# Kernel tuning notes

Measured on AMD Instinct MI355X. Metric: run time of the kernel, lower is better.

Reference implementation:

```python
import jax, jax.numpy as jnp
import numpy as np

BANDWIDTH = 0.001
THRESHOLD_INIT = 0.01


def setup_inputs() -> dict:
    key = jax.random.key(0)
    k1, k2, k3 = jax.random.split(key, 3)
    N, d_model, d_sae = 8192, 2048, 16384
    x = jax.random.normal(k1, (N, d_model), dtype=jnp.float32)
    # scale ~ 1/sqrt(d) so pre-activations are O(1) and threshold=0.01 gives sparsity
    W_enc = jax.random.normal(k2, (d_model, d_sae), dtype=jnp.float32) / np.sqrt(d_model)
    b_enc = jnp.zeros((d_sae,), dtype=jnp.float32)
    threshold = jnp.full((d_sae,), THRESHOLD_INIT, dtype=jnp.float32)
    W_dec = jax.random.normal(k3, (d_sae, d_model), dtype=jnp.float32) / np.sqrt(d_sae)
    b_dec = jnp.zeros((d_model,), dtype=jnp.float32)
    return {"x": x, "W_enc": W_enc, "b_enc": b_enc, "threshold": threshold,
            "W_dec": W_dec, "b_dec": b_dec}


def reference(x, W_enc, b_enc, threshold, W_dec, b_dec):
    # encode: F.linear(x - b_dec, W_enc.t(), b_enc) == (x - b_dec) @ W_enc + b_enc
    pre = (x - b_dec) @ W_enc + b_enc                      # [N, d_sae]
    mask = (pre > threshold).astype(pre.dtype)
    features = pre * mask                                   # JumpReLU
    # decode: features @ W_dec + b_dec
    reconstruction = features @ W_dec + b_dec               # [N, d_model]
    return (reconstruction, features)
```

## Files before the change

kernel.cpp:

```cpp
#include <hip/hip_runtime.h>
#include <hip/hip_bf16.h>


#define BM 128
#define BN 128
#define BK 32

typedef __bf16 bf16x8 __attribute__((ext_vector_type(8)));
typedef float  f32x4  __attribute__((ext_vector_type(4)));

__device__ __forceinline__ short f2bf(float f) {
    unsigned u = __float_as_uint(f);
    unsigned r = u + 0x7FFF + ((u >> 16) & 1);
    return (short)(r >> 16);
}

__device__ __forceinline__ void gl_lds16(const void* g, void* l) {
    __builtin_amdgcn_global_load_lds(
        (const __attribute__((address_space(1))) unsigned int*)g,
        (__attribute__((address_space(3))) unsigned int*)l, 16, 0, 0);
}

__global__ __launch_bounds__(256) void prep_x(const float* __restrict__ x,
                                              const float* __restrict__ b_dec,
                                              short* __restrict__ xb) {
    int idx = (blockIdx.x * 256 + threadIdx.x) * 4;
    float4 v = *(const float4*)(x + idx);
    int k = idx & 2047;
    float4 b = *(const float4*)(b_dec + k);
    short4 o;
    o.x = f2bf(v.x - b.x);
    o.y = f2bf(v.y - b.y);
    o.z = f2bf(v.z - b.z);
    o.w = f2bf(v.w - b.w);
    *(short4*)(xb + idx) = o;
}

__global__ __launch_bounds__(256) void transpose_cvt(const float* __restrict__ in,
                                                     short* __restrict__ out,
                                                     int R, int C) {
    __shared__ float tile[32][33];
    int c0 = blockIdx.x * 32;
    int r0 = blockIdx.y * 32;
    int tx = threadIdx.x, ty = threadIdx.y;
    for (int i = 0; i < 32; i += 8)
        tile[ty + i][tx] = in[(size_t)(r0 + ty + i) * C + (c0 + tx)];
    __syncthreads();
    for (int i = 0; i < 32; i += 8)
        out[(size_t)(c0 + ty + i) * R + (r0 + tx)] = f2bf(tile[tx][ty + i]);
}

__global__ __launch_bounds__(256) void gemm_bt(
    const short* __restrict__ A, const short* __restrict__ Bt,
    const float* __restrict__ bias, const float* __restrict__ thr,
    float* __restrict__ Cf, short* __restrict__ Cb,
    int M, int N, int K) {
    __shared__ short As[BM * BK];
    __shared__ short Bs[BN * BK];

    const int tid  = threadIdx.x;
    const int lane = tid & 63;
    const int wave = tid >> 6;
    const int wm = wave >> 1, wn = wave & 1;
    const int bm = blockIdx.x, bn = blockIdx.y;

    const short* Abase = A  + (size_t)bm * 128 * K;
    const short* Bbase = Bt + (size_t)bn * 128 * K;

    const int srow = lane >> 2;
    const int skof = (lane & 3) * 8;

    f32x4 acc[4][4];
#pragma unroll
    for (int mi = 0; mi < 4; mi++)
#pragma unroll
        for (int ni = 0; ni < 4; ni++)
            acc[mi][ni] = (f32x4){0.f, 0.f, 0.f, 0.f};

    const int mrow = lane & 15;
    const int kq   = (lane >> 4) * 8;

    for (int kt = 0; kt < K; kt += BK) {
#pragma unroll
        for (int i = 0; i < 2; i++) {
            int iid = wave + i * 4;
            int row = iid * 16 + srow;
            gl_lds16(Abase + (size_t)row * K + kt + skof, (char*)As + iid * 1024);
            gl_lds16(Bbase + (size_t)row * K + kt + skof, (char*)Bs + iid * 1024);
        }
        __syncthreads();

        bf16x8 af[4], bfr[4];
#pragma unroll
        for (int mi = 0; mi < 4; mi++)
            af[mi] = *(const bf16x8*)(As + (wm * 64 + mi * 16 + mrow) * BK + kq);
#pragma unroll
        for (int ni = 0; ni < 4; ni++)
            bfr[ni] = *(const bf16x8*)(Bs + (wn * 64 + ni * 16 + mrow) * BK + kq);
#pragma unroll
        for (int mi = 0; mi < 4; mi++)
#pragma unroll
            for (int ni = 0; ni < 4; ni++)
                acc[mi][ni] = __builtin_amdgcn_mfma_f32_16x16x32_bf16(
                    af[mi], bfr[ni], acc[mi][ni], 0, 0, 0);
        __syncthreads();
    }

    const int colbase = bn * 128 + wn * 64;
    const int rowbase = bm * 128 + wm * 64;
#pragma unroll
    for (int mi = 0; mi < 4; mi++) {
        int row0 = rowbase + mi * 16 + (lane >> 4) * 4;
#pragma unroll
        for (int ni = 0; ni < 4; ni++) {
            int col = colbase + ni * 16 + mrow;
            float bz = bias[col];
            float tz = thr ? thr[col] : 0.f;
#pragma unroll
            for (int r = 0; r < 4; r++) {
                float v = acc[mi][ni][r] + bz;
                if (thr) v = (v > tz) ? v : 0.f;
                size_t off = (size_t)(row0 + r) * N + col;
                Cf[off] = v;
                if (Cb) Cb[off] = f2bf(v);
            }
        }
    }
}

extern "C" void kernel_launch(void* const* d_in, const int* in_sizes, int n_in,
                              void* d_out, int out_size, void* d_ws, size_t ws_size,
                              hipStream_t stream) {
    const float* x      = (const float*)d_in[0];
    const float* W_enc  = (const float*)d_in[1];
    const float* b_enc  = (const float*)d_in[2];
    const float* thr    = (const float*)d_in[3];
    const float* W_dec  = (const float*)d_in[4];
    const float* b_dec  = (const float*)d_in[5];

    const int N = 8192, DM = 2048, DS = 16384;

    float* recon = (float*)d_out;
    float* feats = (float*)d_out + (size_t)N * DM;

    char* ws = (char*)d_ws;
    short* xb    = (short*)ws;
    short* wencT = (short*)(ws + ((size_t)32 << 20));
    short* wdecT = (short*)(ws + ((size_t)96 << 20));
    short* fb    = (short*)(ws + ((size_t)160 << 20));

    prep_x<<<(N * DM) / (256 * 4), 256, 0, stream>>>(x, b_dec, xb);
    transpose_cvt<<<dim3(DS / 32, DM / 32), dim3(32, 8), 0, stream>>>(W_enc, wencT, DM, DS);
    transpose_cvt<<<dim3(DM / 32, DS / 32), dim3(32, 8), 0, stream>>>(W_dec, wdecT, DS, DM);

    gemm_bt<<<dim3(N / 128, DS / 128), 256, 0, stream>>>(
        xb, wencT, b_enc, thr, feats, fb, N, DS, DM);
    gemm_bt<<<dim3(N / 128, DM / 128), 256, 0, stream>>>(
        fb, wdecT, b_dec, nullptr, recon, nullptr, N, DM, DS);
}
```

Before: 2.515 ms.

## Replace GEMM with 256x256 double-buffered swizzled 8-wave kernel and faster transpose

Replaces the 128x128 single-buffered GEMM with a 256x256-tile, 512-thread kernel. The new kernel uses a BK=64 double-buffered LDS pipeline, an XOR-swizzled LDS layout, staged prefetch interleaved with four MFMA phases, setprio, and a workgroup remap for L2 locality. The transpose now converts to bf16 before writing to LDS and stores packed short2 values. The aim is more data reuse per tile, hidden global-load latency and fewer LDS bank conflicts. In exchange, the GEMM uses heavy register pressure (one block per CU) and 128KB of LDS.

```diff
diff --git a/kernel.cpp b/kernel.cpp
--- a/kernel.cpp
+++ b/kernel.cpp
@@ -1,10 +1,6 @@
 #include <hip/hip_runtime.h>
 #include <hip/hip_bf16.h>
 
-
-#define BM 128
-#define BN 128
-#define BK 32
 
 typedef __bf16 bf16x8 __attribute__((ext_vector_type(8)));
 typedef float  f32x4  __attribute__((ext_vector_type(4)));
@@ -19,6 +15,12 @@
     __builtin_amdgcn_global_load_lds(
         (const __attribute__((address_space(1))) unsigned int*)g,
         (__attribute__((address_space(3))) unsigned int*)l, 16, 0, 0);
+}
+
+__device__ __forceinline__ void fence_bar() {
+    asm volatile("" ::: "memory");
+    __builtin_amdgcn_s_barrier();
+    asm volatile("" ::: "memory");
 }
 
 __global__ __launch_bounds__(256) void prep_x(const float* __restrict__ x,
@@ -36,91 +38,197 @@
     *(short4*)(xb + idx) = o;
 }
 
-__global__ __launch_bounds__(256) void transpose_cvt(const float* __restrict__ in,
-                                                     short* __restrict__ out,
-                                                     int R, int C) {
-    __shared__ float tile[32][33];
-    int c0 = blockIdx.x * 32;
-    int r0 = blockIdx.y * 32;
-    int tx = threadIdx.x, ty = threadIdx.y;
-    for (int i = 0; i < 32; i += 8)
-        tile[ty + i][tx] = in[(size_t)(r0 + ty + i) * C + (c0 + tx)];
+__global__ __launch_bounds__(256) void transpose_cvt64(const float* __restrict__ in,
+                                                       short* __restrict__ out,
+                                                       int R, int C) {
+    __shared__ short t[32][66];
+    const int tid = threadIdx.x;
+    const int c0 = blockIdx.x * 32;
+    const int r0 = blockIdx.y * 64;
+#pragma unroll
+    for (int i = 0; i < 8; ++i) {
+        int idx = tid + i * 256;
+        int r = idx >> 5, c = idx & 31;
+        t[c][r] = f2bf(in[(size_t)(r0 + r) * C + (c0 + c)]);
+    }
     __syncthreads();
-    for (int i = 0; i < 32; i += 8)
-        out[(size_t)(c0 + ty + i) * R + (r0 + tx)] = f2bf(tile[tx][ty + i]);
-}
-
-__global__ __launch_bounds__(256) void gemm_bt(
+#pragma unroll
+    for (int i = 0; i < 4; ++i) {
+        int idx = tid + i * 256;
+        int orow = idx >> 5, chunk = idx & 31;
+        *(short2*)(&out[(size_t)(c0 + orow) * R + r0 + chunk * 2]) =
+            *(const short2*)(&t[orow][chunk * 2]);
+    }
+}
+
+__global__ __launch_bounds__(512, 1) void gemm256(
     const short* __restrict__ A, const short* __restrict__ Bt,
     const float* __restrict__ bias, const float* __restrict__ thr,
     float* __restrict__ Cf, short* __restrict__ Cb,
     int M, int N, int K) {
-    __shared__ short As[BM * BK];
-    __shared__ short Bs[BN * BK];
+    __shared__ short As[2][256 * 64];
+    __shared__ short Bs[2][256 * 64];
 
     const int tid  = threadIdx.x;
     const int lane = tid & 63;
     const int wave = tid >> 6;
-    const int wm = wave >> 1, wn = wave & 1;
-    const int bm = blockIdx.x, bn = blockIdx.y;
-
-    const short* Abase = A  + (size_t)bm * 128 * K;
-    const short* Bbase = Bt + (size_t)bn * 128 * K;
-
-    const int srow = lane >> 2;
-    const int skof = (lane & 3) * 8;
-
-    f32x4 acc[4][4];
-#pragma unroll
-    for (int mi = 0; mi < 4; mi++)
-#pragma unroll
-        for (int ni = 0; ni < 4; ni++)
-            acc[mi][ni] = (f32x4){0.f, 0.f, 0.f, 0.f};
+    const int wm   = wave >> 2;
+    const int wn   = wave & 3;
+
+    const int Mt   = M >> 8;
+    const int nwg  = gridDim.x * gridDim.y;
+    const int orig = blockIdx.y * gridDim.x + blockIdx.x;
+    const int wg   = (orig & 7) * (nwg >> 3) + (orig >> 3);
+    const int bm   = wg % Mt;
+    const int bn   = wg / Mt;
+
+    const short* Abase = A  + (size_t)bm * 256 * K;
+    const short* Bbase = Bt + (size_t)bn * 256 * K;
+
+    const int srow = tid >> 3;
+    const int csel = ((((tid & 7) << 4) ^ ((srow & 7) << 4)) >> 1);
 
     const int mrow = lane & 15;
-    const int kq   = (lane >> 4) * 8;
-
-    for (int kt = 0; kt < K; kt += BK) {
-#pragma unroll
-        for (int i = 0; i < 2; i++) {
-            int iid = wave + i * 4;
-            int row = iid * 16 + srow;
-            gl_lds16(Abase + (size_t)row * K + kt + skof, (char*)As + iid * 1024);
-            gl_lds16(Bbase + (size_t)row * K + kt + skof, (char*)Bs + iid * 1024);
+    const int hi16 = (lane >> 4) << 4;
+    const int swz  = (mrow & 7) << 4;
+
+    f32x4 acc[8][4];
+#pragma unroll
+    for (int i = 0; i < 8; ++i)
+#pragma unroll
+        for (int j = 0; j < 4; ++j)
+            acc[i][j] = (f32x4){0.f, 0.f, 0.f, 0.f};
+
+    auto stage = [&](int buf, int h, int t) {
+        const short* gb = ((h < 2) ? Abase : Bbase)
+                          + (size_t)((h & 1) * 128 + srow) * K + t * 64 + csel;
+        char* lb = (char*)((h < 2) ? As[buf] : Bs[buf]) + (h & 1) * 16384 + wave * 1024;
+        gl_lds16(gb, lb);
+        gl_lds16(gb + (size_t)64 * K, lb + 8192);
+    };
+
+    const int NT = K >> 6;
+
+    stage(0, 0, 0); stage(0, 1, 0); stage(0, 2, 0); stage(0, 3, 0);
+    stage(1, 0, 1);
+    asm volatile("s_waitcnt vmcnt(2)" ::: "memory");
+    fence_bar();
+
+    bf16x8 af[4][2], bq[2][2];
+
+    for (int t = 0; t < NT; ++t) {
+        const int cur = t & 1, nxt = cur ^ 1;
+        const char* Ard = (const char*)As[cur] + (wm * 128 + mrow) * 128;
+        const char* Brd = (const char*)Bs[cur] + (wn * 64 + mrow) * 128;
+
+#pragma unroll
+        for (int mi = 0; mi < 4; ++mi)
+#pragma unroll
+            for (int kk = 0; kk < 2; ++kk)
+                af[mi][kk] = *(const bf16x8*)(Ard + mi * 2048 + ((kk * 64 + hi16) ^ swz));
+#pragma unroll
+        for (int ni = 0; ni < 2; ++ni)
+#pragma unroll
+            for (int kk = 0; kk < 2; ++kk)
+                bq[ni][kk] = *(const bf16x8*)(Brd + ni * 2048 + ((kk * 64 + hi16) ^ swz));
+        if (t + 1 < NT) stage(nxt, 1, t + 1);
+        fence_bar();
+        asm volatile("s_waitcnt lgkmcnt(0)" ::: "memory");
+        __builtin_amdgcn_s_setprio(1);
+#pragma unroll
+        for (int mi = 0; mi < 4; ++mi)
+#pragma unroll
+            for (int ni = 0; ni < 2; ++ni)
+#pragma unroll
+                for (int kk = 0; kk < 2; ++kk)
+                    acc[mi][ni] = __builtin_amdgcn_mfma_f32_16x16x32_bf16(
+                        af[mi][kk], bq[ni][kk], acc[mi][ni], 0, 0, 0);
+        __builtin_amdgcn_s_setprio(0);
+        fence_bar();
+
+#pragma unroll
+        for (int ni = 0; ni < 2; ++ni)
+#pragma unroll
+            for (int kk = 0; kk < 2; ++kk)
+                bq[ni][kk] = *(const bf16x8*)(Brd + (2 + ni) * 2048 + ((kk * 64 + hi16) ^ swz));
+        if (t + 1 < NT) stage(nxt, 2, t + 1);
+        fence_bar();
+        asm volatile("s_waitcnt lgkmcnt(0)" ::: "memory");
+        __builtin_amdgcn_s_setprio(1);
+#pragma unroll
+        for (int mi = 0; mi < 4; ++mi)
+#pragma unroll
+            for (int ni = 0; ni < 2; ++ni)
+#pragma unroll
+                for (int kk = 0; kk < 2; ++kk)
+                    acc[mi][2 + ni] = __builtin_amdgcn_mfma_f32_16x16x32_bf16(
+                        af[mi][kk], bq[ni][kk], acc[mi][2 + ni], 0, 0, 0);
+        __builtin_amdgcn_s_setprio(0);
+        fence_bar();
+
+#pragma unroll
+        for (int mi = 0; mi < 4; ++mi)
+#pragma unroll
+            for (int kk = 0; kk < 2; ++kk)
+                af[mi][kk] = *(const bf16x8*)(Ard + (4 + mi) * 2048 + ((kk * 64 + hi16) ^ swz));
+        if (t + 1 < NT) stage(nxt, 3, t + 1);
+        fence_bar();
+        asm volatile("s_waitcnt lgkmcnt(0)" ::: "memory");
+        __builtin_amdgcn_s_setprio(1);
+#pragma unroll
+        for (int mi = 0; mi < 4; ++mi)
+#pragma unroll
+            for (int ni = 0; ni < 2; ++ni)
+#pragma unroll
+                for (int kk = 0; kk < 2; ++kk)
+                    acc[4 + mi][2 + ni] = __builtin_amdgcn_mfma_f32_16x16x32_bf16(
+                        af[mi][kk], bq[ni][kk], acc[4 + mi][2 + ni], 0, 0, 0);
+        __builtin_amdgcn_s_setprio(0);
+        fence_bar();
+
+#pragma unroll
+        for (int ni = 0; ni < 2; ++ni)
+#pragma unroll
+            for (int kk = 0; kk < 2; ++kk)
+                bq[ni][kk] = *(const bf16x8*)(Brd + ni * 2048 + ((kk * 64 + hi16) ^ swz));
+        if (t + 2 < NT) stage(cur, 0, t + 2);
+        fence_bar();
+        asm volatile("s_waitcnt lgkmcnt(0)" ::: "memory");
+        __builtin_amdgcn_s_setprio(1);
+#pragma unroll
+        for (int mi = 0; mi < 4; ++mi)
+#pragma unroll
+            for (int ni = 0; ni < 2; ++ni)
+#pragma unroll
+                for (int kk = 0; kk < 2; ++kk)
+                    acc[4 + mi][ni] = __builtin_amdgcn_mfma_f32_16x16x32_bf16(
+                        af[mi][kk], bq[ni][kk], acc[4 + mi][ni], 0, 0, 0);
+        __builtin_amdgcn_s_setprio(0);
+        if (t + 2 < NT) {
+            asm volatile("s_waitcnt vmcnt(2)" ::: "memory");
+        } else if (t + 1 < NT) {
+            asm volatile("s_waitcnt vmcnt(0)" ::: "memory");
         }
-        __syncthreads();
-
-        bf16x8 af[4], bfr[4];
-#pragma unroll
-        for (int mi = 0; mi < 4; mi++)
-            af[mi] = *(const bf16x8*)(As + (wm * 64 + mi * 16 + mrow) * BK + kq);
-#pragma unroll
-        for (int ni = 0; ni < 4; ni++)
-            bfr[ni] = *(const bf16x8*)(Bs + (wn * 64 + ni * 16 + mrow) * BK + kq);
-#pragma unroll
-        for (int mi = 0; mi < 4; mi++)
-#pragma unroll
-            for (int ni = 0; ni < 4; ni++)
-                acc[mi][ni] = __builtin_amdgcn_mfma_f32_16x16x32_bf16(
-                    af[mi], bfr[ni], acc[mi][ni], 0, 0, 0);
-        __syncthreads();
-    }
-
-    const int colbase = bn * 128 + wn * 64;
-    const int rowbase = bm * 128 + wm * 64;
-#pragma unroll
-    for (int mi = 0; mi < 4; mi++) {
-        int row0 = rowbase + mi * 16 + (lane >> 4) * 4;
-#pragma unroll
-        for (int ni = 0; ni < 4; ni++) {
-            int col = colbase + ni * 16 + mrow;
-            float bz = bias[col];
-            float tz = thr ? thr[col] : 0.f;
-#pragma unroll
-            for (int r = 0; r < 4; r++) {
-                float v = acc[mi][ni][r] + bz;
-                if (thr) v = (v > tz) ? v : 0.f;
-                size_t off = (size_t)(row0 + r) * N + col;
+        fence_bar();
+    }
+
+    const int colb = bn * 256 + wn * 64 + mrow;
+    const int rowb = bm * 256 + wm * 128 + ((lane >> 4) << 2);
+    float bz[4], tz[4];
+#pragma unroll
+    for (int ni = 0; ni < 4; ++ni) {
+        bz[ni] = bias[colb + ni * 16];
+        tz[ni] = thr ? thr[colb + ni * 16] : 0.f;
+    }
+#pragma unroll
+    for (int mi = 0; mi < 8; ++mi) {
+#pragma unroll
+        for (int ni = 0; ni < 4; ++ni) {
+#pragma unroll
+            for (int r = 0; r < 4; ++r) {
+                float v = acc[mi][ni][r] + bz[ni];
+                if (thr) v = (v > tz[ni]) ? v : 0.f;
+                size_t off = (size_t)(rowb + mi * 16 + r) * N + colb + ni * 16;
                 Cf[off] = v;
                 if (Cb) Cb[off] = f2bf(v);
             }
@@ -150,11 +258,11 @@
     short* fb    = (short*)(ws + ((size_t)160 << 20));
 
     prep_x<<<(N * DM) / (256 * 4), 256, 0, stream>>>(x, b_dec, xb);
-    transpose_cvt<<<dim3(DS / 32, DM / 32), dim3(32, 8), 0, stream>>>(W_enc, wencT, DM, DS);
-    transpose_cvt<<<dim3(DM / 32, DS / 32), dim3(32, 8), 0, stream>>>(W_dec, wdecT, DS, DM);
-
-    gemm_bt<<<dim3(N / 128, DS / 128), 256, 0, stream>>>(
+    transpose_cvt64<<<dim3(DS / 32, DM / 64), 256, 0, stream>>>(W_enc, wencT, DM, DS);
+    transpose_cvt64<<<dim3(DM / 32, DS / 64), 256, 0, stream>>>(W_dec, wdecT, DS, DM);
+
+    gemm256<<<dim3(N / 256, DS / 256), 512, 0, stream>>>(
         xb, wencT, b_enc, thr, feats, fb, N, DS, DM);
-    gemm_bt<<<dim3(N / 128, DM / 128), 256, 0, stream>>>(
+    gemm256<<<dim3(N / 256, DM / 256), 512, 0, stream>>>(
         fb, wdecT, b_dec, nullptr, recon, nullptr, N, DM, DS);
 }
```

After: 2.342 ms. 1.07x faster.
